# Optimization experiments

Hardware: AMD Instinct MI355X
Metric: run time of the kernel (lower is better)

Reference implementation:

```python
import jax, jax.numpy as jnp
import numpy as np

N = 50000      # nodes
E = 1600000    # edges (before self loops)
B = 512        # graphs
D = 128        # gcn dim (constant across the 3 GAT layers)
H = 1024       # hidden_dim
O = 128        # output_dim
NEG_SLOPE = 0.2


def setup_inputs() -> dict:
    key = jax.random.key(0)
    ks = jax.random.split(key, 24)
    inp = {
        "x": jax.random.normal(ks[0], (N, D), jnp.float32),
        "edge_index": jax.random.randint(ks[1], (2, E), 0, N, dtype=jnp.int64),
        "edge_weight": jax.random.uniform(ks[2], (E,), jnp.float32),
        "batch": jnp.sort(jax.random.randint(ks[3], (N,), 0, B, dtype=jnp.int64)),
    }
    s = 1.0 / np.sqrt(D)
    for i in range(3):
        k = 4 + 4 * i
        inp[f"W{i+1}"] = jax.random.normal(ks[k], (D, D), jnp.float32) * s
        inp[f"as{i+1}"] = jax.random.normal(ks[k + 1], (D,), jnp.float32) * s
        inp[f"ad{i+1}"] = jax.random.normal(ks[k + 2], (D,), jnp.float32) * s
        inp[f"b{i+1}"] = jnp.zeros((D,), jnp.float32)
    inp["Wf1"] = jax.random.normal(ks[16], (D, H), jnp.float32) * s
    inp["bf1"] = jnp.zeros((H,), jnp.float32)
    inp["Wf2"] = jax.random.normal(ks[17], (H, O), jnp.float32) * (1.0 / np.sqrt(H))
    inp["bf2"] = jnp.zeros((O,), jnp.float32)
    return inp


def gat_conv(x, src, dst, W, a_src, a_dst, b):
    """PyG GATConv, heads=1: gather -> leakyrelu -> segment softmax -> scatter-add."""
    h = x @ W                                   # [N, D]
    e = jax.nn.leaky_relu(jnp.take(h @ a_src, src) + jnp.take(h @ a_dst, dst), NEG_SLOPE)  # [E']
    m = jax.ops.segment_max(e, dst, num_segments=N)
    ex = jnp.exp(e - m[dst])
    denom = jax.ops.segment_sum(ex, dst, num_segments=N)
    alpha = ex / denom[dst]                      # segment softmax over incoming edges
    out = jax.ops.segment_sum(alpha[:, None] * h[src], dst, num_segments=N)
    return out + b


def reference(x, edge_index, edge_weight, batch,
              W1, as1, ad1, b1, W2, as2, ad2, b2, W3, as3, ad3, b3,
              Wf1, bf1, Wf2, bf2):
    # GATConv adds self loops; edge_weight is unused by GATConv (faithful to original)
    loop = jnp.arange(N, dtype=edge_index.dtype)
    src = jnp.concatenate([edge_index[0], loop])
    dst = jnp.concatenate([edge_index[1], loop])

    h = gat_conv(x, src, dst, W1, as1, ad1, b1)
    h = jax.nn.relu(gat_conv(h, src, dst, W2, as2, ad2, b2))
    h = jax.nn.relu(gat_conv(h, src, dst, W3, as3, ad3, b3))

    # global mean pool (gep)
    sums = jax.ops.segment_sum(h, batch, num_segments=B)        # [B, D]
    counts = jax.ops.segment_sum(jnp.ones((N,), h.dtype), batch, num_segments=B)
    pooled = sums / jnp.maximum(counts, 1.0)[:, None]

    # MLP head; dropout is identity at inference
    o = jax.nn.relu(pooled) @ Wf1 + bf1
    o = jax.nn.relu(o) @ Wf2 + bf2
    return o
```

## Files before the change

### kernel.cpp

```cpp
#include <hip/hip_runtime.h>
#include <cstdint>
#include <cstddef>

#define NEG_SLOPE 0.2f

typedef _Float16 f16x8 __attribute__((ext_vector_type(8)));
typedef float f32x4v __attribute__((ext_vector_type(4)));

__device__ __forceinline__ unsigned enc_f(float f) {
  unsigned u = __float_as_uint(f);
  return (u & 0x80000000u) ? ~u : (u | 0x80000000u);
}
__device__ __forceinline__ float dec_f(unsigned u) {
  return (u & 0x80000000u) ? __uint_as_float(u ^ 0x80000000u) : __uint_as_float(~u);
}

#define AST 136
#define WST 136
#define HST 132
#define SMEM_BYTES (64 * AST * 2 + 128 * WST * 2)

__global__ void k_bounds(const int* __restrict__ batch, int N, int B,
                         int* __restrict__ gstart, unsigned* __restrict__ maxPart,
                         int* __restrict__ counts) {
  int n = blockIdx.x * blockDim.x + threadIdx.x;
  if (n < 768) maxPart[n] = 0u;
  if (n >= N) return;
  counts[n] = 0;
  int cur = batch[n];
  if (n == 0) {
    for (int g = 0; g <= cur; g++) gstart[g] = 0;
  } else {
    int prev = batch[n - 1];
    for (int g = prev + 1; g <= cur; g++) gstart[g] = n;
  }
  if (n == N - 1) {
    for (int g = cur + 1; g <= B; g++) gstart[g] = N;
  }
}

__global__ void k_count_rank(const int* __restrict__ dst, int E,
                             int* counts, int* __restrict__ rank) {
  int e = blockIdx.x * blockDim.x + threadIdx.x;
  if (e < E) rank[e] = atomicAdd(&counts[dst[e]], 1);
}

__global__ __launch_bounds__(1024) void k_scan1(const int* __restrict__ counts, int N,
                                                int* __restrict__ row_ptr, int* __restrict__ part) {
  __shared__ int tmp[1024];
  int t = threadIdx.x;
  int i = blockIdx.x * 1024 + t;
  int v = (i < N) ? 1 + counts[i] : 0;
  tmp[t] = v;
  __syncthreads();
  for (int off = 1; off < 1024; off <<= 1) {
    int u = (t >= off) ? tmp[t - off] : 0;
    __syncthreads();
    tmp[t] += u;
    __syncthreads();
  }
  if (i < N) row_ptr[i + 1] = tmp[t];
  if (t == 1023) part[blockIdx.x] = tmp[t];
}

__global__ __launch_bounds__(1024) void k_scan3(int* __restrict__ row_ptr,
                                                const int* __restrict__ part, int N) {
  __shared__ int s_off;
  int bi = blockIdx.x;
  if (threadIdx.x == 0) {
    int run = 0;
    for (int b = 0; b < bi; b++) run += part[b];
    s_off = run;
    if (bi == 0) row_ptr[0] = 0;
  }
  __syncthreads();
  int i = bi * 1024 + threadIdx.x;
  if (i < N) row_ptr[i + 1] += s_off;
}

__device__ __forceinline__ void gemm_body(char* smem, float* redmax, int bx,
                                          const float* __restrict__ A32,
                                          const unsigned short* __restrict__ A16,
                                          const float* __restrict__ W,
                                          unsigned short* __restrict__ hb,
                                          const float* __restrict__ asrc,
                                          const float* __restrict__ adst,
                                          float* __restrict__ sv, float* __restrict__ dv,
                                          unsigned* __restrict__ maxSlot, int M) {
  _Float16* Ah = (_Float16*)smem;
  _Float16* Wt = (_Float16*)(smem + 64 * AST * 2);
  float*    hS = (float*)(smem + 64 * AST * 2);
  int t = threadIdx.x;
  int rowbase = bx * 64;

  if (A16) {
    for (int i = t; i < 64 * 16; i += 256) {
      int r = i >> 4, c8 = (i & 15) << 3;
      int gr = rowbase + r;
      uint4 v = make_uint4(0u, 0u, 0u, 0u);
      if (gr < M) v = *(const uint4*)&A16[(size_t)gr * 128 + c8];
      *(uint4*)&Ah[r * AST + c8] = v;
    }
  } else {
    for (int i = t; i < 64 * 32; i += 256) {
      int r = i >> 5, c4 = (i & 31) << 2;
      int gr = rowbase + r;
      float4 v = make_float4(0.f, 0.f, 0.f, 0.f);
      if (gr < M) v = *(const float4*)&A32[(size_t)gr * 128 + c4];
      _Float16 tmp[4] = {(_Float16)v.x, (_Float16)v.y, (_Float16)v.z, (_Float16)v.w};
      *(short4*)&Ah[r * AST + c4] = *(short4*)tmp;
    }
  }
  for (int i = t; i < 128 * 32; i += 256) {
    int r = i >> 5, c4 = (i & 31) << 2;
    float4 v = *(const float4*)&W[(size_t)r * 128 + c4];
    Wt[(c4 + 0) * WST + r] = (_Float16)v.x;
    Wt[(c4 + 1) * WST + r] = (_Float16)v.y;
    Wt[(c4 + 2) * WST + r] = (_Float16)v.z;
    Wt[(c4 + 3) * WST + r] = (_Float16)v.w;
  }
  __syncthreads();

  int wave = t >> 6, lane = t & 63, quad = lane >> 4, l15 = lane & 15;
  f32x4v acc[4][2];
#pragma unroll
  for (int mt = 0; mt < 4; mt++)
#pragma unroll
    for (int nt = 0; nt < 2; nt++) {
      acc[mt][nt][0] = 0.f; acc[mt][nt][1] = 0.f; acc[mt][nt][2] = 0.f; acc[mt][nt][3] = 0.f;
    }

#pragma unroll
  for (int s = 0; s < 4; s++) {
    int k0 = (s << 5) + (quad << 3);
    f16x8 af[4], bf[2];
#pragma unroll
    for (int mt = 0; mt < 4; mt++)
      af[mt] = *(f16x8*)&Ah[(mt * 16 + l15) * AST + k0];
#pragma unroll
    for (int nt = 0; nt < 2; nt++)
      bf[nt] = *(f16x8*)&Wt[(wave * 32 + nt * 16 + l15) * WST + k0];
#pragma unroll
    for (int mt = 0; mt < 4; mt++)
#pragma unroll
      for (int nt = 0; nt < 2; nt++)
        acc[mt][nt] = __builtin_amdgcn_mfma_f32_16x16x32_f16(af[mt], bf[nt], acc[mt][nt], 0, 0, 0);
  }
  __syncthreads();

#pragma unroll
  for (int mt = 0; mt < 4; mt++)
#pragma unroll
    for (int nt = 0; nt < 2; nt++)
#pragma unroll
      for (int rr = 0; rr < 4; rr++)
        hS[(mt * 16 + quad * 4 + rr) * HST + wave * 32 + nt * 16 + l15] = acc[mt][nt][rr];
  __syncthreads();

  int tx = t & 31, ty = t >> 5;
  float4 av  = *(const float4*)&asrc[tx * 4];
  float4 adv = *(const float4*)&adst[tx * 4];
  float wmax = -1e30f;
#pragma unroll
  for (int r8 = 0; r8 < 8; r8++) {
    int row = r8 * 8 + ty;
    int gr = rowbase + row;
    float4 hv = *(float4*)&hS[row * HST + tx * 4];
    float ps = hv.x * av.x + hv.y * av.y + hv.z * av.z + hv.w * av.w;
    float pd = hv.x * adv.x + hv.y * adv.y + hv.z * adv.z + hv.w * adv.w;
#pragma unroll
    for (int mask = 16; mask; mask >>= 1) {
      ps += __shfl_xor(ps, mask);
      pd += __shfl_xor(pd, mask);
    }
    if (gr < M) {
      _Float16 hq[4] = {(_Float16)hv.x, (_Float16)hv.y, (_Float16)hv.z, (_Float16)hv.w};
      *(uint2*)&hb[(size_t)gr * 128 + tx * 4] = *(uint2*)hq;
      if (tx == 0) { sv[gr] = ps; dv[gr] = pd; wmax = fmaxf(wmax, ps); }
    }
  }
#pragma unroll
  for (int mask = 32; mask; mask >>= 1) wmax = fmaxf(wmax, __shfl_xor(wmax, mask));
  if ((t & 63) == 0) redmax[t >> 6] = wmax;
  __syncthreads();
  if (t == 0) {
    float mx = fmaxf(fmaxf(redmax[0], redmax[1]), fmaxf(redmax[2], redmax[3]));
    atomicMax(&maxSlot[bx & 255], enc_f(mx));
  }
}

__global__ __launch_bounds__(256) void k_fill_gemm(const int* __restrict__ src,
                                                   const int* __restrict__ dst,
                                                   const int* __restrict__ rank, int E, int N,
                                                   const int* __restrict__ row_ptr,
                                                   int* __restrict__ col,
                                                   const float* __restrict__ A32,
                                                   const float* __restrict__ W,
                                                   unsigned short* __restrict__ hb,
                                                   const float* __restrict__ asrc,
                                                   const float* __restrict__ adst,
                                                   float* __restrict__ sv, float* __restrict__ dv,
                                                   unsigned* __restrict__ maxSlot, int Gg) {
  __shared__ __align__(16) char smem[SMEM_BYTES];
  __shared__ float redmax[4];
  int b = (int)blockIdx.x;
  bool isGemm = ((b % 9) == 4) && ((b / 9) < Gg);
  if (isGemm) {
    gemm_body(smem, redmax, b / 9, A32, (const unsigned short*)nullptr, W,
              hb, asrc, adst, sv, dv, maxSlot, N);
  } else {
    int nGemmBefore = (b >= 4) ? min((b - 4) / 9 + 1, Gg) : 0;
    int i = (b - nGemmBefore) * 256 + threadIdx.x;
    if (i < N) col[row_ptr[i]] = i;
    int e = i - N;
    if (e >= 0 && e < E) col[row_ptr[dst[e]] + 1 + rank[e]] = src[e];
  }
}

__global__ __launch_bounds__(256) void k_gemm_fused(const unsigned short* __restrict__ A16,
                                                    const float* __restrict__ W,
                                                    unsigned short* __restrict__ hb,
                                                    const float* __restrict__ asrc,
                                                    const float* __restrict__ adst,
                                                    float* __restrict__ sv, float* __restrict__ dv,
                                                    unsigned* __restrict__ maxSlot, int M) {
  __shared__ __align__(16) char smem[SMEM_BYTES];
  __shared__ float redmax[4];
  gemm_body(smem, redmax, (int)blockIdx.x, (const float*)nullptr, A16, W,
            hb, asrc, adst, sv, dv, maxSlot, M);
}

__global__ __launch_bounds__(256) void k_agg(const unsigned short* __restrict__ hb,
                                             const float* __restrict__ sv,
                                             const float* __restrict__ dv,
                                             const int* __restrict__ row_ptr,
                                             const int* __restrict__ col,
                                             const float* __restrict__ bias,
                                             const unsigned* __restrict__ maxSlot,
                                             unsigned short* __restrict__ out16,
                                             int N, int relu) {
  int wid = (int)((blockIdx.x * (size_t)blockDim.x + threadIdx.x) >> 6);
  int lane = threadIdx.x & 63;
  if (wid >= N) return;

  unsigned mp = max(max(maxSlot[lane], maxSlot[lane + 64]),
                    max(maxSlot[lane + 128], maxSlot[lane + 192]));
#pragma unroll
  for (int off = 32; off; off >>= 1) mp = max(mp, __shfl_xor(mp, off));
  float maxS = dec_f(mp);

  int beg = row_ptr[wid], end = row_ptr[wid + 1];
  float dn = dv[wid];
  float m = maxS + dn;
  m = (m > 0.f) ? m : NEG_SLOPE * m;

  int g = lane >> 4, sub = lane & 15;
  const uint32_t* hbu = (const uint32_t*)hb;
  float acc[8];
#pragma unroll
  for (int k = 0; k < 8; k++) acc[k] = 0.f;
  float dsum = 0.f;

#define FETCH_SLOT(K, W, H)                                                \
  {                                                                        \
    int sl = ((K) << 2) + g;                                               \
    int sn = __shfl(sn_l, sl);                                             \
    W = __shfl(w_l, sl);                                                   \
    H = make_uint4(0u, 0u, 0u, 0u);                                        \
    if (sl < cnt) H = *(const uint4*)(hbu + (size_t)sn * 64 + sub * 4);    \
  }
#define ACC_SLOT(W, H)                                                     \
  {                                                                        \
    const _Float16* hp = (const _Float16*)&H;                              \
    _Pragma("unroll")                                                      \
    for (int q = 0; q < 8; q++) acc[q] += W * (float)hp[q];                \
  }

  for (int base = beg; base < end; base += 64) {
    int cnt = min(end - base, 64);

    int sn_l = 0;
    float w_l = 0.f;
    if (lane < cnt) {
      sn_l = col[base + lane];
      float e = sv[sn_l] + dn;
      e = (e > 0.f) ? e : NEG_SLOPE * e;
      w_l = __expf(e - m);
      dsum += w_l;
    }

    int kmaxW = (cnt + 3) >> 2;
    float wA, wB, wC, wD;
    uint4 hA, hB, hC, hD;
    FETCH_SLOT(0, wA, hA);
    FETCH_SLOT(1, wB, hB);
    FETCH_SLOT(2, wC, hC);
    for (int k = 3; k < kmaxW; k++) {
      FETCH_SLOT(k, wD, hD);
      ACC_SLOT(wA, hA);
      wA = wB; hA = hB;
      wB = wC; hB = hC;
      wC = wD; hC = hD;
    }
    ACC_SLOT(wA, hA);
    ACC_SLOT(wB, hB);
    ACC_SLOT(wC, hC);
  }

#pragma unroll
  for (int off = 1; off < 64; off <<= 1) dsum += __shfl_xor(dsum, off);
#pragma unroll
  for (int k = 0; k < 8; k++) {
    acc[k] += __shfl_xor(acc[k], 16);
    acc[k] += __shfl_xor(acc[k], 32);
  }
  if (lane < 16) {
    float inv = 1.f / dsum;
    float o[8];
    const float* bp = &bias[sub * 8];
#pragma unroll
    for (int k = 0; k < 8; k++) {
      o[k] = acc[k] * inv + bp[k];
      if (relu) o[k] = fmaxf(o[k], 0.f);
    }
    _Float16 q[8];
#pragma unroll
    for (int k = 0; k < 8; k++) q[k] = (_Float16)o[k];
    *(uint4*)&out16[(size_t)wid * 128 + sub * 8] = *(uint4*)q;
  }
}

__global__ __launch_bounds__(256) void k_pool(const unsigned short* __restrict__ h16,
                                              const int* __restrict__ gstart,
                                              float* __restrict__ pooled, int B) {
  __shared__ float red[4][128];
  int b = blockIdx.x, t = threadIdx.x;
  int c = t & 63, seg = t >> 6;
  int s0 = gstart[b], s1 = gstart[b + 1];
  int cnt = s1 - s0;
  int per = (cnt + 3) >> 2;
  int n0 = s0 + seg * per;
  int n1 = min(n0 + per, s1);
  const uint32_t* hu = (const uint32_t*)h16;
  float a0 = 0.f, a1 = 0.f;
  for (int n = n0; n < n1; n++) {
    union { uint32_t u; _Float16 h[2]; } cv;
    cv.u = hu[(size_t)n * 64 + c];
    a0 += (float)cv.h[0];
    a1 += (float)cv.h[1];
  }
  if (seg) { red[seg][2 * c] = a0; red[seg][2 * c + 1] = a1; }
  __syncthreads();
  if (seg == 0) {
    a0 += red[1][2 * c] + red[2][2 * c] + red[3][2 * c];
    a1 += red[1][2 * c + 1] + red[2][2 * c + 1] + red[3][2 * c + 1];
    float inv = 1.f / (float)(cnt > 0 ? cnt : 1);
    pooled[b * 128 + 2 * c]     = fmaxf(a0 * inv, 0.f);
    pooled[b * 128 + 2 * c + 1] = fmaxf(a1 * inv, 0.f);
  }
}

__global__ __launch_bounds__(256) void k_mlp(const float* __restrict__ pooled,
                                             const float* __restrict__ Wf1,
                                             const float* __restrict__ bf1,
                                             const float* __restrict__ Wf2,
                                             const float* __restrict__ bf2,
                                             float* __restrict__ out, int B) {
  __shared__ float P[4][128];
  __shared__ float H1[4][1024];
  __shared__ float R[4][128];
  int t = threadIdx.x;
  int g0 = blockIdx.x * 4;

  for (int i = t; i < 4 * 128; i += 256) {
    int gi = i >> 7, c = i & 127;
    P[gi][c] = (g0 + gi < B) ? pooled[(size_t)(g0 + gi) * 128 + c] : 0.f;
  }
  __syncthreads();

#pragma unroll
  for (int cb = 0; cb < 4; cb++) {
    int c = cb * 256 + t;
    float a0 = 0.f, a1 = 0.f, a2 = 0.f, a3 = 0.f;
    for (int k = 0; k < 128; k++) {
      float w = Wf1[(size_t)k * 1024 + c];
      a0 += P[0][k] * w; a1 += P[1][k] * w; a2 += P[2][k] * w; a3 += P[3][k] * w;
    }
    float b = bf1[c];
    H1[0][c] = fmaxf(a0 + b, 0.f);
    H1[1][c] = fmaxf(a1 + b, 0.f);
    H1[2][c] = fmaxf(a2 + b, 0.f);
    H1[3][c] = fmaxf(a3 + b, 0.f);
  }
  __syncthreads();

  int c = t & 127, hh = t >> 7;
  float a0 = 0.f, a1 = 0.f, a2 = 0.f, a3 = 0.f;
  int k0 = hh * 512;
  for (int k = k0; k < k0 + 512; k++) {
    float w = Wf2[(size_t)k * 128 + c];
    a0 += H1[0][k] * w; a1 += H1[1][k] * w; a2 += H1[2][k] * w; a3 += H1[3][k] * w;
  }
  if (hh == 1) { R[0][c] = a0; R[1][c] = a1; R[2][c] = a2; R[3][c] = a3; }
  __syncthreads();
  if (hh == 0) {
    float b = bf2[c];
    float o0 = a0 + R[0][c] + b;
    float o1 = a1 + R[1][c] + b;
    float o2 = a2 + R[2][c] + b;
    float o3 = a3 + R[3][c] + b;
    if (g0 + 0 < B) out[(size_t)(g0 + 0) * 128 + c] = o0;
    if (g0 + 1 < B) out[(size_t)(g0 + 1) * 128 + c] = o1;
    if (g0 + 2 < B) out[(size_t)(g0 + 2) * 128 + c] = o2;
    if (g0 + 3 < B) out[(size_t)(g0 + 3) * 128 + c] = o3;
  }
}

extern "C" void kernel_launch(void* const* d_in, const int* in_sizes, int n_in,
                              void* d_out, int out_size, void* d_ws, size_t ws_size,
                              hipStream_t stream) {
  const float* x     = (const float*)d_in[0];
  const int*   ei    = (const int*)d_in[1];
  const int*   batch = (const int*)d_in[3];
  const float* W1 = (const float*)d_in[4];
  const float* as1 = (const float*)d_in[5];
  const float* ad1 = (const float*)d_in[6];
  const float* b1 = (const float*)d_in[7];
  const float* W2 = (const float*)d_in[8];
  const float* as2 = (const float*)d_in[9];
  const float* ad2 = (const float*)d_in[10];
  const float* b2 = (const float*)d_in[11];
  const float* W3 = (const float*)d_in[12];
  const float* as3 = (const float*)d_in[13];
  const float* ad3 = (const float*)d_in[14];
  const float* b3 = (const float*)d_in[15];
  const float* Wf1 = (const float*)d_in[16];
  const float* bf1 = (const float*)d_in[17];
  const float* Wf2 = (const float*)d_in[18];
  const float* bf2 = (const float*)d_in[19];

  const int N = in_sizes[0] / 128;
  const int E = in_sizes[1] / 2;
  const int B = out_size / 128;

  char* base_ws = (char*)d_ws;
  size_t off = 0;
  auto carve = [&](size_t bytes) -> void* {
    off = (off + 255) & ~(size_t)255;
    void* p = base_ws + off;
    off += bytes;
    return p;
  };
  int* counts   = (int*)carve((size_t)N * 4);
  int* row_ptr  = (int*)carve((size_t)(N + 1) * 4);
  int* rank     = (int*)carve((size_t)E * 4);
  int* col      = (int*)carve((size_t)(E + N) * 4);
  int* part     = (int*)carve(1024 * 4);
  int* gstart   = (int*)carve((size_t)(B + 1) * 4);
  unsigned* maxPart = (unsigned*)carve(768 * 4);
  float* sbuf   = (float*)carve((size_t)N * 4);
  float* dbuf   = (float*)carve((size_t)N * 4);
  unsigned short* hb  = (unsigned short*)carve((size_t)N * 128 * 2);
  unsigned short* a16 = (unsigned short*)carve((size_t)N * 128 * 2);
  float* pooled = (float*)carve((size_t)B * 128 * 4);

  const int* srcp = ei;
  const int* dstp = ei + E;
  const int nb = (N + 1023) / 1024;
  const int Gg = (N + 63) / 64;
  const int Gf = (E + N + 255) / 256;

  hipLaunchKernelGGL(k_bounds, dim3((N + 255) / 256), dim3(256), 0, stream,
                     batch, N, B, gstart, maxPart, counts);
  hipLaunchKernelGGL(k_count_rank, dim3((E + 255) / 256), dim3(256), 0, stream,
                     dstp, E, counts, rank);
  hipLaunchKernelGGL(k_scan1, dim3(nb), dim3(1024), 0, stream, counts, N, row_ptr, part);
  hipLaunchKernelGGL(k_scan3, dim3(nb), dim3(1024), 0, stream, row_ptr, part, N);

  hipLaunchKernelGGL(k_fill_gemm, dim3(Gf + Gg), dim3(256), 0, stream,
                     srcp, dstp, rank, E, N, row_ptr, col,
                     x, W1, hb, as1, ad1, sbuf, dbuf, maxPart + 0 * 256, Gg);

  hipLaunchKernelGGL(k_agg, dim3((N + 3) / 4), dim3(256), 0, stream,
                     hb, sbuf, dbuf, row_ptr, col, b1, maxPart + 0 * 256, a16, N, 0);

  hipLaunchKernelGGL(k_gemm_fused, dim3(Gg), dim3(256), 0, stream,
                     a16, W2, hb, as2, ad2, sbuf, dbuf, maxPart + 1 * 256, N);
  hipLaunchKernelGGL(k_agg, dim3((N + 3) / 4), dim3(256), 0, stream,
                     hb, sbuf, dbuf, row_ptr, col, b2, maxPart + 1 * 256, a16, N, 1);

  hipLaunchKernelGGL(k_gemm_fused, dim3(Gg), dim3(256), 0, stream,
                     a16, W3, hb, as3, ad3, sbuf, dbuf, maxPart + 2 * 256, N);
  hipLaunchKernelGGL(k_agg, dim3((N + 3) / 4), dim3(256), 0, stream,
                     hb, sbuf, dbuf, row_ptr, col, b3, maxPart + 2 * 256, a16, N, 1);

  hipLaunchKernelGGL(k_pool, dim3(B), dim3(256), 0, stream, a16, gstart, pooled, B);
  hipLaunchKernelGGL(k_mlp, dim3((B + 3) / 4), dim3(256), 0, stream,
                     pooled, Wf1, bf1, Wf2, bf2, (float*)d_out, B);
}
```

Baseline: 522.3 us.

## Pretranspose weights once, fuse layer-1 GEMM with edge counting, deepen agg prefetch

Each of the three weight matrices is converted to a transposed fp16 copy once in a prep block, so every GEMM block no longer converts and transposes W into shared memory. The B fragments are now read directly from global memory. The attention dot products are computed from the MFMA accumulators using shuffles plus a small shared reduction, and the fp32 staging tile is replaced by an fp16 one. The layer-1 GEMM now overlaps with the edge-count atomics instead of the CSR fill, which becomes its own kernel. The aggregation prefetch pipeline goes from 3 to 5 slots, at the cost of more registers and more global B-fragment loads per block.

```diff
diff --git a/kernel.cpp b/kernel.cpp
--- a/kernel.cpp
+++ b/kernel.cpp
@@ -16,14 +16,37 @@
 }
 
 #define AST 136
-#define WST 136
-#define HST 132
-#define SMEM_BYTES (64 * AST * 2 + 128 * WST * 2)
-
-__global__ void k_bounds(const int* __restrict__ batch, int N, int B,
-                         int* __restrict__ gstart, unsigned* __restrict__ maxPart,
-                         int* __restrict__ counts) {
-  int n = blockIdx.x * blockDim.x + threadIdx.x;
+#define ABYTES (64 * AST * 2)
+#define SMEM_BYTES (ABYTES + 4 * 64 * 2 * 4)
+
+__global__ void k_bounds_prep(const int* __restrict__ batch, int N, int B,
+                              int* __restrict__ gstart, unsigned* __restrict__ maxPart,
+                              int* __restrict__ counts,
+                              const float* __restrict__ W1, const float* __restrict__ W2,
+                              const float* __restrict__ W3,
+                              _Float16* __restrict__ Wt1, _Float16* __restrict__ Wt2,
+                              _Float16* __restrict__ Wt3, int nbb) {
+  int b = blockIdx.x;
+  if (b >= nbb) {
+    int wi = b - nbb;
+    const float* W = (wi == 0) ? W1 : (wi == 1) ? W2 : W3;
+    _Float16* Wt = (wi == 0) ? Wt1 : (wi == 1) ? Wt2 : Wt3;
+    for (int i = threadIdx.x; i < 2048; i += 256) {
+      int k = i >> 4, n8 = (i & 15) << 3;
+      float4 v0 = *(const float4*)&W[(size_t)k * 128 + n8];
+      float4 v1 = *(const float4*)&W[(size_t)k * 128 + n8 + 4];
+      Wt[(size_t)(n8 + 0) * 128 + k] = (_Float16)v0.x;
+      Wt[(size_t)(n8 + 1) * 128 + k] = (_Float16)v0.y;
+      Wt[(size_t)(n8 + 2) * 128 + k] = (_Float16)v0.z;
+      Wt[(size_t)(n8 + 3) * 128 + k] = (_Float16)v0.w;
+      Wt[(size_t)(n8 + 4) * 128 + k] = (_Float16)v1.x;
+      Wt[(size_t)(n8 + 5) * 128 + k] = (_Float16)v1.y;
+      Wt[(size_t)(n8 + 6) * 128 + k] = (_Float16)v1.z;
+      Wt[(size_t)(n8 + 7) * 128 + k] = (_Float16)v1.w;
+    }
+    return;
+  }
+  int n = b * blockDim.x + threadIdx.x;
   if (n < 768) maxPart[n] = 0u;
   if (n >= N) return;
   counts[n] = 0;
@@ -39,12 +62,6 @@
   }
 }
 
-__global__ void k_count_rank(const int* __restrict__ dst, int E,
-                             int* counts, int* __restrict__ rank) {
-  int e = blockIdx.x * blockDim.x + threadIdx.x;
-  if (e < E) rank[e] = atomicAdd(&counts[dst[e]], 1);
-}
-
 __global__ __launch_bounds__(1024) void k_scan1(const int* __restrict__ counts, int N,
                                                 int* __restrict__ row_ptr, int* __restrict__ part) {
   __shared__ int tmp[1024];
@@ -78,18 +95,17 @@
   if (i < N) row_ptr[i + 1] += s_off;
 }
 
-__device__ __forceinline__ void gemm_body(char* smem, float* redmax, int bx,
+__device__ __forceinline__ void gemm_body(char* smem, int bx,
                                           const float* __restrict__ A32,
                                           const unsigned short* __restrict__ A16,
-                                          const float* __restrict__ W,
+                                          const _Float16* __restrict__ WtG,
                                           unsigned short* __restrict__ hb,
                                           const float* __restrict__ asrc,
                                           const float* __restrict__ adst,
                                           float* __restrict__ sv, float* __restrict__ dv,
                                           unsigned* __restrict__ maxSlot, int M) {
   _Float16* Ah = (_Float16*)smem;
-  _Float16* Wt = (_Float16*)(smem + 64 * AST * 2);
-  float*    hS = (float*)(smem + 64 * AST * 2);
+  float (*sred)[64][2] = (float (*)[64][2])(smem + ABYTES);
   int t = threadIdx.x;
   int rowbase = bx * 64;
 
@@ -111,14 +127,6 @@
       *(short4*)&Ah[r * AST + c4] = *(short4*)tmp;
     }
   }
-  for (int i = t; i < 128 * 32; i += 256) {
-    int r = i >> 5, c4 = (i & 31) << 2;
-    float4 v = *(const float4*)&W[(size_t)r * 128 + c4];
-    Wt[(c4 + 0) * WST + r] = (_Float16)v.x;
-    Wt[(c4 + 1) * WST + r] = (_Float16)v.y;
-    Wt[(c4 + 2) * WST + r] = (_Float16)v.z;
-    Wt[(c4 + 3) * WST + r] = (_Float16)v.w;
-  }
   __syncthreads();
 
   int wave = t >> 6, lane = t & 63, quad = lane >> 4, l15 = lane & 15;
@@ -139,7 +147,7 @@
       af[mt] = *(f16x8*)&Ah[(mt * 16 + l15) * AST + k0];
 #pragma unroll
     for (int nt = 0; nt < 2; nt++)
-      bf[nt] = *(f16x8*)&Wt[(wave * 32 + nt * 16 + l15) * WST + k0];
+      bf[nt] = *(const f16x8*)&WtG[(size_t)(wave * 32 + nt * 16 + l15) * 128 + k0];
 #pragma unroll
     for (int mt = 0; mt < 4; mt++)
 #pragma unroll
@@ -148,85 +156,91 @@
   }
   __syncthreads();
 
-#pragma unroll
-  for (int mt = 0; mt < 4; mt++)
-#pragma unroll
-    for (int nt = 0; nt < 2; nt++)
-#pragma unroll
-      for (int rr = 0; rr < 4; rr++)
-        hS[(mt * 16 + quad * 4 + rr) * HST + wave * 32 + nt * 16 + l15] = acc[mt][nt][rr];
+  float avv0 = asrc[wave * 32 + l15],      avv1 = asrc[wave * 32 + 16 + l15];
+  float adv0 = adst[wave * 32 + l15],      adv1 = adst[wave * 32 + 16 + l15];
+  _Float16* hS16 = (_Float16*)smem;
+#pragma unroll
+  for (int mt = 0; mt < 4; mt++) {
+#pragma unroll
+    for (int rr = 0; rr < 4; rr++) {
+      int row = mt * 16 + quad * 4 + rr;
+      hS16[row * AST + wave * 32 + l15]      = (_Float16)acc[mt][0][rr];
+      hS16[row * AST + wave * 32 + 16 + l15] = (_Float16)acc[mt][1][rr];
+      float ps = acc[mt][0][rr] * avv0 + acc[mt][1][rr] * avv1;
+      float pd = acc[mt][0][rr] * adv0 + acc[mt][1][rr] * adv1;
+#pragma unroll
+      for (int mask = 8; mask; mask >>= 1) {
+        ps += __shfl_xor(ps, mask);
+        pd += __shfl_xor(pd, mask);
+      }
+      if (l15 == 0) { sred[wave][row][0] = ps; sred[wave][row][1] = pd; }
+    }
+  }
   __syncthreads();
 
   int tx = t & 31, ty = t >> 5;
-  float4 av  = *(const float4*)&asrc[tx * 4];
-  float4 adv = *(const float4*)&adst[tx * 4];
-  float wmax = -1e30f;
 #pragma unroll
   for (int r8 = 0; r8 < 8; r8++) {
     int row = r8 * 8 + ty;
     int gr = rowbase + row;
-    float4 hv = *(float4*)&hS[row * HST + tx * 4];
-    float ps = hv.x * av.x + hv.y * av.y + hv.z * av.z + hv.w * av.w;
-    float pd = hv.x * adv.x + hv.y * adv.y + hv.z * adv.z + hv.w * adv.w;
-#pragma unroll
-    for (int mask = 16; mask; mask >>= 1) {
-      ps += __shfl_xor(ps, mask);
-      pd += __shfl_xor(pd, mask);
-    }
-    if (gr < M) {
-      _Float16 hq[4] = {(_Float16)hv.x, (_Float16)hv.y, (_Float16)hv.z, (_Float16)hv.w};
-      *(uint2*)&hb[(size_t)gr * 128 + tx * 4] = *(uint2*)hq;
-      if (tx == 0) { sv[gr] = ps; dv[gr] = pd; wmax = fmaxf(wmax, ps); }
-    }
-  }
-#pragma unroll
-  for (int mask = 32; mask; mask >>= 1) wmax = fmaxf(wmax, __shfl_xor(wmax, mask));
-  if ((t & 63) == 0) redmax[t >> 6] = wmax;
-  __syncthreads();
-  if (t == 0) {
-    float mx = fmaxf(fmaxf(redmax[0], redmax[1]), fmaxf(redmax[2], redmax[3]));
-    atomicMax(&maxSlot[bx & 255], enc_f(mx));
-  }
-}
-
-__global__ __launch_bounds__(256) void k_fill_gemm(const int* __restrict__ src,
-                                                   const int* __restrict__ dst,
-                                                   const int* __restrict__ rank, int E, int N,
-                                                   const int* __restrict__ row_ptr,
-                                                   int* __restrict__ col,
-                                                   const float* __restrict__ A32,
-                                                   const float* __restrict__ W,
-                                                   unsigned short* __restrict__ hb,
-                                                   const float* __restrict__ asrc,
-                                                   const float* __restrict__ adst,
-                                                   float* __restrict__ sv, float* __restrict__ dv,
-                                                   unsigned* __restrict__ maxSlot, int Gg) {
+    if (gr < M)
+      *(uint2*)&hb[(size_t)gr * 128 + tx * 4] = *(const uint2*)&hS16[row * AST + tx * 4];
+  }
+
+  if (t < 64) {
+    int gr = rowbase + t;
+    float ps = sred[0][t][0] + sred[1][t][0] + sred[2][t][0] + sred[3][t][0];
+    float pd = sred[0][t][1] + sred[1][t][1] + sred[2][t][1] + sred[3][t][1];
+    float wmax = -1e30f;
+    if (gr < M) { sv[gr] = ps; dv[gr] = pd; wmax = ps; }
+#pragma unroll
+    for (int mask = 32; mask; mask >>= 1) wmax = fmaxf(wmax, __shfl_xor(wmax, mask));
+    if (t == 0) atomicMax(&maxSlot[bx & 255], enc_f(wmax));
+  }
+}
+
+__global__ __launch_bounds__(256) void k_count_gemm(const int* __restrict__ dst, int E,
+                                                    int* counts, int* __restrict__ rank,
+                                                    const float* __restrict__ A32,
+                                                    const _Float16* __restrict__ WtG,
+                                                    unsigned short* __restrict__ hb,
+                                                    const float* __restrict__ asrc,
+                                                    const float* __restrict__ adst,
+                                                    float* __restrict__ sv, float* __restrict__ dv,
+                                                    unsigned* __restrict__ maxSlot, int Gg, int N) {
   __shared__ __align__(16) char smem[SMEM_BYTES];
-  __shared__ float redmax[4];
   int b = (int)blockIdx.x;
-  bool isGemm = ((b % 9) == 4) && ((b / 9) < Gg);
+  bool isGemm = ((b & 7) == 4) && ((b >> 3) < Gg);
   if (isGemm) {
-    gemm_body(smem, redmax, b / 9, A32, (const unsigned short*)nullptr, W,
+    gemm_body(smem, b >> 3, A32, (const unsigned short*)nullptr, WtG,
               hb, asrc, adst, sv, dv, maxSlot, N);
   } else {
-    int nGemmBefore = (b >= 4) ? min((b - 4) / 9 + 1, Gg) : 0;
-    int i = (b - nGemmBefore) * 256 + threadIdx.x;
-    if (i < N) col[row_ptr[i]] = i;
-    int e = i - N;
-    if (e >= 0 && e < E) col[row_ptr[dst[e]] + 1 + rank[e]] = src[e];
-  }
+    int nGemmBefore = (b >= 4) ? min(((b - 4) >> 3) + 1, Gg) : 0;
+    int e = (b - nGemmBefore) * 256 + threadIdx.x;
+    if (e < E) rank[e] = atomicAdd(&counts[dst[e]], 1);
+  }
+}
+
+__global__ __launch_bounds__(256) void k_fill(const int* __restrict__ src,
+                                              const int* __restrict__ dst,
+                                              const int* __restrict__ rank, int E, int N,
+                                              const int* __restrict__ row_ptr,
+                                              int* __restrict__ col) {
+  int i = blockIdx.x * 256 + threadIdx.x;
+  if (i < N) col[row_ptr[i]] = i;
+  int e = i - N;
+  if (e >= 0 && e < E) col[row_ptr[dst[e]] + 1 + rank[e]] = src[e];
 }
 
 __global__ __launch_bounds__(256) void k_gemm_fused(const unsigned short* __restrict__ A16,
-                                                    const float* __restrict__ W,
+                                                    const _Float16* __restrict__ WtG,
                                                     unsigned short* __restrict__ hb,
                                                     const float* __restrict__ asrc,
                                                     const float* __restrict__ adst,
                                                     float* __restrict__ sv, float* __restrict__ dv,
                                                     unsigned* __restrict__ maxSlot, int M) {
   __shared__ __align__(16) char smem[SMEM_BYTES];
-  __shared__ float redmax[4];
-  gemm_body(smem, redmax, (int)blockIdx.x, (const float*)nullptr, A16, W,
+  gemm_body(smem, (int)blockIdx.x, (const float*)nullptr, A16, WtG,
             hb, asrc, adst, sv, dv, maxSlot, M);
 }
 
@@ -290,21 +304,27 @@
     }
 
     int kmaxW = (cnt + 3) >> 2;
-    float wA, wB, wC, wD;
-    uint4 hA, hB, hC, hD;
+    float wA, wB, wC, wD, wE, wF;
+    uint4 hA, hB, hC, hD, hE, hF;
     FETCH_SLOT(0, wA, hA);
     FETCH_SLOT(1, wB, hB);
     FETCH_SLOT(2, wC, hC);
-    for (int k = 3; k < kmaxW; k++) {
-      FETCH_SLOT(k, wD, hD);
+    FETCH_SLOT(3, wD, hD);
+    FETCH_SLOT(4, wE, hE);
+    for (int k = 5; k < kmaxW; k++) {
+      FETCH_SLOT(k, wF, hF);
       ACC_SLOT(wA, hA);
       wA = wB; hA = hB;
       wB = wC; hB = hC;
       wC = wD; hC = hD;
+      wD = wE; hD = hE;
+      wE = wF; hE = hF;
     }
     ACC_SLOT(wA, hA);
     ACC_SLOT(wB, hB);
     ACC_SLOT(wC, hC);
+    ACC_SLOT(wD, hD);
+    ACC_SLOT(wE, hE);
   }
 
 #pragma unroll
@@ -463,34 +483,42 @@
   unsigned short* hb  = (unsigned short*)carve((size_t)N * 128 * 2);
   unsigned short* a16 = (unsigned short*)carve((size_t)N * 128 * 2);
   float* pooled = (float*)carve((size_t)B * 128 * 4);
+  _Float16* Wt1 = (_Float16*)carve(128 * 128 * 2);
+  _Float16* Wt2 = (_Float16*)carve(128 * 128 * 2);
+  _Float16* Wt3 = (_Float16*)carve(128 * 128 * 2);
 
   const int* srcp = ei;
   const int* dstp = ei + E;
   const int nb = (N + 1023) / 1024;
   const int Gg = (N + 63) / 64;
+  const int Cb = (E + 255) / 256;
   const int Gf = (E + N + 255) / 256;
-
-  hipLaunchKernelGGL(k_bounds, dim3((N + 255) / 256), dim3(256), 0, stream,
-                     batch, N, B, gstart, maxPart, counts);
-  hipLaunchKernelGGL(k_count_rank, dim3((E + 255) / 256), dim3(256), 0, stream,
-                     dstp, E, counts, rank);
+  const int nbb = (N + 255) / 256;
+
+  hipLaunchKernelGGL(k_bounds_prep, dim3(nbb + 3), dim3(256), 0, stream,
+                     batch, N, B, gstart, maxPart, counts,
+                     W1, W2, W3, Wt1, Wt2, Wt3, nbb);
+
+  hipLaunchKernelGGL(k_count_gemm, dim3(Cb + Gg), dim3(256), 0, stream,
+                     dstp, E, counts, rank,
+                     x, Wt1, hb, as1, ad1, sbuf, dbuf, maxPart + 0 * 256, Gg, N);
+
   hipLaunchKernelGGL(k_scan1, dim3(nb), dim3(1024), 0, stream, counts, N, row_ptr, part);
   hipLaunchKernelGGL(k_scan3, dim3(nb), dim3(1024), 0, stream, row_ptr, part, N);
 
-  hipLaunchKernelGGL(k_fill_gemm, dim3(Gf + Gg), dim3(256), 0, stream,
-                     srcp, dstp, rank, E, N, row_ptr, col,
-                     x, W1, hb, as1, ad1, sbuf, dbuf, maxPart + 0 * 256, Gg);
+  hipLaunchKernelGGL(k_fill, dim3(Gf), dim3(256), 0, stream,
+                     srcp, dstp, rank, E, N, row_ptr, col);
 
   hipLaunchKernelGGL(k_agg, dim3((N + 3) / 4), dim3(256), 0, stream,
                      hb, sbuf, dbuf, row_ptr, col, b1, maxPart + 0 * 256, a16, N, 0);
 
   hipLaunchKernelGGL(k_gemm_fused, dim3(Gg), dim3(256), 0, stream,
-                     a16, W2, hb, as2, ad2, sbuf, dbuf, maxPart + 1 * 256, N);
+                     a16, Wt2, hb, as2, ad2, sbuf, dbuf, maxPart + 1 * 256, N);
   hipLaunchKernelGGL(k_agg, dim3((N + 3) / 4), dim3(256), 0, stream,
                      hb, sbuf, dbuf, row_ptr, col, b2, maxPart + 1 * 256, a16, N, 1);
 
   hipLaunchKernelGGL(k_gemm_fused, dim3(Gg), dim3(256), 0, stream,
-                     a16, W3, hb, as3, ad3, sbuf, dbuf, maxPart + 2 * 256, N);
+                     a16, Wt3, hb, as3, ad3, sbuf, dbuf, maxPart + 2 * 256, N);
   hipLaunchKernelGGL(k_agg, dim3((N + 3) / 4), dim3(256), 0, stream,
                      hb, sbuf, dbuf, row_ptr, col, b3, maxPart + 2 * 256, a16, N, 1);
 
```

After: 525.6 us. Within noise of the previous version (+0.6%).
